# Optimization experiments

Hardware: AMD Instinct MI355X
Metric: run time of the kernel (lower is better)

Reference implementation:

```python
import jax, jax.numpy as jnp
import numpy as np
from jax import lax

DIM = 128
HEADS = 8
B, H, W = 8, 128, 128


def conv1x1(w, x):
    # w: [out_c, in_c], x: [b, in_c, h, w]
    return jnp.einsum('oc,bchw->bohw', w, x)


def setup_inputs() -> dict:
    key = jax.random.key(0)
    ks = jax.random.split(key, 12)
    s = 0.02
    return {
        'x': jax.random.normal(ks[0], (B, DIM, H, W), dtype=jnp.float32),
        'W_qkv': jax.random.normal(ks[1], (3 * DIM, DIM), dtype=jnp.float32) * s,
        'W_dw': jax.random.normal(ks[2], (DIM, 1, 3, 3), dtype=jnp.float32) * s,
        'W_proj_s': jax.random.normal(ks[3], (DIM, DIM), dtype=jnp.float32) * s,
        'scale_s': jnp.ones((HEADS, 1, 1), dtype=jnp.float32),
        'W_ff1': jax.random.normal(ks[4], (DIM, DIM), dtype=jnp.float32) * s,
        'W_ff2': jax.random.normal(ks[5], (DIM, DIM), dtype=jnp.float32) * s,
        'W_proj_f': jax.random.normal(ks[6], (DIM, DIM), dtype=jnp.float32) * s,
        'W_gsf': jax.random.normal(ks[7], (DIM, DIM), dtype=jnp.float32) * s,
        'b_gsf': jnp.zeros((DIM,), dtype=jnp.float32),
        'W_gfs': jax.random.normal(ks[8], (DIM, DIM), dtype=jnp.float32) * s,
        'b_gfs': jnp.zeros((DIM,), dtype=jnp.float32),
    }


def reference(x, W_qkv, W_dw, W_proj_s, scale_s, W_ff1, W_ff2, W_proj_f,
              W_gsf, b_gsf, W_gfs, b_gfs):
    b, c, h, w = x.shape
    head = HEADS
    ch = c // head

    # --- channel self-attention branch ---
    qkv = conv1x1(W_qkv, x)                      # [b, 3c, h, w]
    q_s, k_s, v_s = jnp.split(qkv, 3, axis=1)
    v_s_conv = lax.conv_general_dilated(
        v_s, W_dw, window_strides=(1, 1), padding='SAME',
        feature_group_count=c,
        dimension_numbers=('NCHW', 'OIHW', 'NCHW'))  # depthwise 3x3

    q = q_s.reshape(b, head, ch, h * w)
    k = k_s.reshape(b, head, ch, h * w)
    v = v_s.reshape(b, head, ch, h * w)
    attn = jax.nn.softmax(jnp.einsum('bhcn,bhdn->bhcd', q, k) * scale_s, axis=-1)
    out_s = jnp.einsum('bhcd,bhdn->bhcn', attn, v).reshape(b, c, h, w)
    out_s = conv1x1(W_proj_s, out_s + v_s_conv)

    # --- frequency filter branch ---
    xf = jnp.fft.rfft2(x, norm='ortho')          # complex [b,c,h,w//2+1]
    spatial_weights = conv1x1(W_ff2, jax.nn.gelu(conv1x1(W_ff1, x), approximate=False))
    freq_weights = jnp.fft.rfft2(spatial_weights, norm='ortho')
    out_f = jnp.fft.irfft2(xf * freq_weights, s=(h, w), norm='ortho')
    out_f = conv1x1(W_proj_f, out_f)

    # --- sigmoid-gated fusion ---
    gate_f = jax.nn.sigmoid(conv1x1(W_gsf, out_s) + b_gsf[:, None, None])
    gate_s = jax.nn.sigmoid(conv1x1(W_gfs, out_f) + b_gfs[:, None, None])
    return x + out_s * gate_s + out_f * gate_f
```

## Files before the change

kernel.cpp:

```cpp
#include <hip/hip_runtime.h>
#include <hip/hip_bf16.h>
#include <math.h>

#define HW 16384

typedef __attribute__((ext_vector_type(8))) short bf16x8;
typedef __attribute__((ext_vector_type(4))) float f32x4;

__device__ __forceinline__ unsigned short f2bf(float a)
{
    __hip_bfloat16 h = __float2bfloat16(a);
    return __builtin_bit_cast(unsigned short, h);
}
__device__ __forceinline__ unsigned f2bf_pk(float a, float b)
{
    return (unsigned)f2bf(a) | ((unsigned)f2bf(b) << 16);
}
__device__ __forceinline__ float bf2f(unsigned short u)
{
    return __uint_as_float(((unsigned)u) << 16);
}
__device__ __forceinline__ float sigmoidf_(float v) { return 1.f / (1.f + expf(-v)); }

__device__ __forceinline__ float2 cmul(float2 a, float2 b)
{
    return make_float2(a.x * b.x - a.y * b.y, a.x * b.y + a.y * b.x);
}

__global__ __launch_bounds__(256)
void wprep_k(const float* __restrict__ w0, const float* __restrict__ w1,
             const float* __restrict__ w2, const float* __restrict__ w3,
             const float* __restrict__ w4, const float* __restrict__ w5,
             const float* __restrict__ w6, int4* __restrict__ Wbf4)
{
    int m = blockIdx.x >> 3;
    int slot = (blockIdx.x & 7) * 256 + threadIdx.x;
    const float* src;
    switch (m) {
        case 0: src = w0; break;
        case 1: src = w1; break;
        case 2: src = w2; break;
        case 3: src = w3; break;
        case 4: src = w4; break;
        case 5: src = w5; break;
        default: src = w6; break;
    }
    int o = slot >> 4;
    int c16 = (slot & 15) ^ (o & 7);
    const float* p = src + o * 128 + c16 * 8;
    int4 pk;
    pk.x = f2bf_pk(p[0], p[1]); pk.y = f2bf_pk(p[2], p[3]);
    pk.z = f2bf_pk(p[4], p[5]); pk.w = f2bf_pk(p[6], p[7]);
    Wbf4[m * 2048 + slot] = pk;
}

__global__ __launch_bounds__(256)
void head_k(const float* __restrict__ x, const int4* __restrict__ wv,
            const int4* __restrict__ w1, const int4* __restrict__ w2,
            unsigned short* __restrict__ V, unsigned short* __restrict__ swb,
            unsigned short* __restrict__ xb)
{
    __shared__ short WL[128 * 128];
    __shared__ short XLx[64 * 128];
    __shared__ short XM[64 * 128];
    int t = threadIdx.x;
    int gb = blockIdx.x;
    int b = gb >> 8;
    int n0 = (gb & 255) << 6;

    #pragma unroll
    for (int it = 0; it < 8; ++it)
        ((int4*)WL)[it * 256 + t] = wv[it * 256 + t];

    const float* inb = x + (size_t)b * 128 * HW + n0;
    int nl = t & 63;
    #pragma unroll
    for (int it = 0; it < 4; ++it) {
        int c8 = (t >> 6) + it * 4;
        float v[8];
        unsigned short vb[8];
        #pragma unroll
        for (int j = 0; j < 8; ++j) {
            v[j] = inb[(size_t)(c8 * 8 + j) * HW + nl];
            vb[j] = f2bf(v[j]);
            xb[((size_t)(b * 128) + c8 * 8 + j) * HW + n0 + nl] = vb[j];
        }
        int4 p;
        p.x = (int)((unsigned)vb[0] | ((unsigned)vb[1] << 16));
        p.y = (int)((unsigned)vb[2] | ((unsigned)vb[3] << 16));
        p.z = (int)((unsigned)vb[4] | ((unsigned)vb[5] << 16));
        p.w = (int)((unsigned)vb[6] | ((unsigned)vb[7] << 16));
        ((int4*)XLx)[nl * 16 + (c8 ^ (nl & 7))] = p;
    }
    __syncthreads();

    int l = t & 63, w = t >> 6, kg = l >> 4, l15 = l & 15, l7 = l15 & 7;

    f32x4 acc[2][4];
    #pragma unroll
    for (int mf = 0; mf < 2; ++mf)
        #pragma unroll
        for (int nf = 0; nf < 4; ++nf) acc[mf][nf] = (f32x4){0.f, 0.f, 0.f, 0.f};
    #pragma unroll
    for (int ks = 0; ks < 4; ++ks) {
        int ch = ks * 4 + kg;
        bf16x8 A0 = ((const bf16x8*)WL)[(w * 32 + l15) * 16 + (ch ^ l7)];
        bf16x8 A1 = ((const bf16x8*)WL)[(w * 32 + 16 + l15) * 16 + (ch ^ l7)];
        #pragma unroll
        for (int nf = 0; nf < 4; ++nf) {
            bf16x8 Bf = ((const bf16x8*)XLx)[(nf * 16 + l15) * 16 + (ch ^ l7)];
            acc[0][nf] = __builtin_amdgcn_mfma_f32_16x16x32_bf16(A0, Bf, acc[0][nf], 0, 0, 0);
            acc[1][nf] = __builtin_amdgcn_mfma_f32_16x16x32_bf16(A1, Bf, acc[1][nf], 0, 0, 0);
        }
    }
    #pragma unroll
    for (int mf = 0; mf < 2; ++mf)
        #pragma unroll
        for (int nf = 0; nf < 4; ++nf)
            #pragma unroll
            for (int i = 0; i < 4; ++i) {
                int row = w * 32 + mf * 16 + kg * 4 + i;
                int col = n0 + nf * 16 + l15;
                V[((size_t)b * 128 + row) * HW + col] = f2bf(acc[mf][nf][i]);
            }
    __syncthreads();

    #pragma unroll
    for (int it = 0; it < 8; ++it)
        ((int4*)WL)[it * 256 + t] = w1[it * 256 + t];
    __syncthreads();

    #pragma unroll
    for (int mf = 0; mf < 2; ++mf)
        #pragma unroll
        for (int nf = 0; nf < 4; ++nf) acc[mf][nf] = (f32x4){0.f, 0.f, 0.f, 0.f};
    #pragma unroll
    for (int ks = 0; ks < 4; ++ks) {
        int ch = ks * 4 + kg;
        bf16x8 A0 = ((const bf16x8*)WL)[(w * 32 + l15) * 16 + (ch ^ l7)];
        bf16x8 A1 = ((const bf16x8*)WL)[(w * 32 + 16 + l15) * 16 + (ch ^ l7)];
        #pragma unroll
        for (int nf = 0; nf < 4; ++nf) {
            bf16x8 Bf = ((const bf16x8*)XLx)[(nf * 16 + l15) * 16 + (ch ^ l7)];
            acc[0][nf] = __builtin_amdgcn_mfma_f32_16x16x32_bf16(A0, Bf, acc[0][nf], 0, 0, 0);
            acc[1][nf] = __builtin_amdgcn_mfma_f32_16x16x32_bf16(A1, Bf, acc[1][nf], 0, 0, 0);
        }
    }
    __syncthreads();

    #pragma unroll
    for (int it = 0; it < 8; ++it)
        ((int4*)WL)[it * 256 + t] = w2[it * 256 + t];
    #pragma unroll
    for (int mf = 0; mf < 2; ++mf)
        #pragma unroll
        for (int nf = 0; nf < 4; ++nf) {
            float g4[4];
            #pragma unroll
            for (int i = 0; i < 4; ++i) {
                float v = acc[mf][nf][i];
                g4[i] = 0.5f * v * (1.0f + erff(v * 0.70710678118654752f));
            }
            int col = nf * 16 + l15;
            int r0 = w * 32 + mf * 16 + kg * 4;
            int octet = r0 >> 3;
            uint2 pk2;
            pk2.x = f2bf_pk(g4[0], g4[1]);
            pk2.y = f2bf_pk(g4[2], g4[3]);
            ((uint2*)XM)[(col * 16 + (octet ^ (col & 7))) * 2 + (kg & 1)] = pk2;
        }
    __syncthreads();

    f32x4 acc2[2][4];
    #pragma unroll
    for (int mf = 0; mf < 2; ++mf)
        #pragma unroll
        for (int nf = 0; nf < 4; ++nf) acc2[mf][nf] = (f32x4){0.f, 0.f, 0.f, 0.f};
    #pragma unroll
    for (int ks = 0; ks < 4; ++ks) {
        int ch = ks * 4 + kg;
        bf16x8 A0 = ((const bf16x8*)WL)[(w * 32 + l15) * 16 + (ch ^ l7)];
        bf16x8 A1 = ((const bf16x8*)WL)[(w * 32 + 16 + l15) * 16 + (ch ^ l7)];
        #pragma unroll
        for (int nf = 0; nf < 4; ++nf) {
            bf16x8 Bf = ((const bf16x8*)XM)[(nf * 16 + l15) * 16 + (ch ^ l7)];
            acc2[0][nf] = __builtin_amdgcn_mfma_f32_16x16x32_bf16(A0, Bf, acc2[0][nf], 0, 0, 0);
            acc2[1][nf] = __builtin_amdgcn_mfma_f32_16x16x32_bf16(A1, Bf, acc2[1][nf], 0, 0, 0);
        }
    }
    #pragma unroll
    for (int mf = 0; mf < 2; ++mf)
        #pragma unroll
        for (int nf = 0; nf < 4; ++nf)
            #pragma unroll
            for (int i = 0; i < 4; ++i) {
                int row = w * 32 + mf * 16 + kg * 4 + i;
                int col = n0 + nf * 16 + l15;
                swb[((size_t)b * 128 + row) * HW + col] = f2bf(acc2[mf][nf][i]);
            }
}

__global__ __launch_bounds__(256)
void dwconv_k(const unsigned short* __restrict__ V, const float* __restrict__ Wdw,
              unsigned short* __restrict__ vcb)
{
    __shared__ unsigned short Vt[128 * 128];
    int t = threadIdx.x;
    int bc = blockIdx.x;
    int c = bc & 127;
    const unsigned short* vin = V + (size_t)bc * HW;
    #pragma unroll
    for (int i = 0; i < 16; ++i) {
        int idx = i * 256 + t;
        ((uint2*)Vt)[idx] = ((const uint2*)vin)[idx];
    }
    float wf[9];
    #pragma unroll
    for (int i = 0; i < 9; ++i) wf[i] = Wdw[c * 9 + i];
    __syncthreads();
    #pragma unroll
    for (int i = 0; i < 16; ++i) {
        int q = i * 256 + t;
        int y = q >> 5;
        int x0 = (q & 31) << 2;
        float a0 = 0.f, a1 = 0.f, a2 = 0.f, a3 = 0.f;
        #pragma unroll
        for (int dy = 0; dy < 3; ++dy) {
            int yy = y + dy - 1;
            if (yy < 0 || yy > 127) continue;
            const unsigned short* r = Vt + yy * 128;
            uint2 mu = *(const uint2*)(r + x0);
            float m0 = bf2f((unsigned short)(mu.x & 0xFFFF));
            float m1 = bf2f((unsigned short)(mu.x >> 16));
            float m2 = bf2f((unsigned short)(mu.y & 0xFFFF));
            float m3 = bf2f((unsigned short)(mu.y >> 16));
            float left  = (x0 > 0)   ? bf2f(r[x0 - 1]) : 0.f;
            float right = (x0 < 124) ? bf2f(r[x0 + 4]) : 0.f;
            float w0 = wf[dy * 3], w1 = wf[dy * 3 + 1], w2 = wf[dy * 3 + 2];
            a0 += w0 * left + w1 * m0 + w2 * m1;
            a1 += w0 * m0   + w1 * m1 + w2 * m2;
            a2 += w0 * m1   + w1 * m2 + w2 * m3;
            a3 += w0 * m2   + w1 * m3 + w2 * right;
        }
        uint2 r2;
        r2.x = f2bf_pk(a0, a1);
        r2.y = f2bf_pk(a2, a3);
        *(uint2*)(vcb + (size_t)bc * HW + y * 128 + x0) = r2;
    }
}

__global__ __launch_bounds__(256)
void gram_mfma_k(const unsigned short* __restrict__ xb, float* __restrict__ Gp)
{
    __shared__ short XL[128 * 128];
    int t = threadIdx.x;
    int blk = blockIdx.x;
    int b = blk >> 5, ks = blk & 31;
    const unsigned short* xbb = xb + (size_t)b * 128 * HW + ks * 512;
    int l = t & 63, w = t >> 6, kg = l >> 4, l15 = l & 15, l7 = l15 & 7;

    f32x4 acc[2][8];
    #pragma unroll
    for (int mf = 0; mf < 2; ++mf)
        #pragma unroll
        for (int nf = 0; nf < 8; ++nf) acc[mf][nf] = (f32x4){0.f, 0.f, 0.f, 0.f};

    for (int kc = 0; kc < 4; ++kc) {
        __syncthreads();
        #pragma unroll
        for (int it = 0; it < 8; ++it) {
            int g = it * 256 + t;
            int row = g >> 4, oct = g & 15;
            ((int4*)XL)[row * 16 + (oct ^ (row & 7))] =
                *(const int4*)(xbb + (size_t)row * HW + kc * 128 + oct * 8);
        }
        __syncthreads();
        #pragma unroll
        for (int s = 0; s < 4; ++s) {
            int oct = s * 4 + kg;
            bf16x8 A0 = ((const bf16x8*)XL)[(w * 32 + l15) * 16 + (oct ^ l7)];
            bf16x8 A1 = ((const bf16x8*)XL)[(w * 32 + 16 + l15) * 16 + (oct ^ l7)];
            #pragma unroll
            for (int nf = 0; nf < 8; ++nf) {
                bf16x8 Bf = ((const bf16x8*)XL)[(nf * 16 + l15) * 16 + (oct ^ l7)];
                acc[0][nf] = __builtin_amdgcn_mfma_f32_16x16x32_bf16(A0, Bf, acc[0][nf], 0, 0, 0);
                acc[1][nf] = __builtin_amdgcn_mfma_f32_16x16x32_bf16(A1, Bf, acc[1][nf], 0, 0, 0);
            }
        }
    }
    float* gp = Gp + (size_t)blk * 16384;
    #pragma unroll
    for (int mf = 0; mf < 2; ++mf)
        #pragma unroll
        for (int nf = 0; nf < 8; ++nf)
            #pragma unroll
            for (int i = 0; i < 4; ++i) {
                int row = w * 32 + mf * 16 + kg * 4 + i;
                int col = nf * 16 + l15;
                gp[row * 128 + col] = acc[mf][nf][i];
            }
}

__global__ void gram_reduce_k(const float* __restrict__ Gp, float* __restrict__ G)
{
    int idx = blockIdx.x * 256 + threadIdx.x;
    int b = idx >> 14;
    int ij = idx & 16383;
    const float* gp = Gp + (size_t)(b * 32) * 16384 + ij;
    float s = 0.f;
    #pragma unroll
    for (int ks = 0; ks < 32; ++ks) s += gp[(size_t)ks * 16384];
    G[idx] = s;
}

__global__ __launch_bounds__(256)
void attn_s2_k(const float* __restrict__ G, const float* __restrict__ Wqkv,
               const float* __restrict__ scale, float* __restrict__ S)
{
    __shared__ float Wq[16][129];
    __shared__ float Wk[16][129];
    __shared__ float Ts[16][129];
    int bh = blockIdx.x;
    int b = bh >> 3, h = bh & 7;
    int t = threadIdx.x;
    #pragma unroll
    for (int i = 0; i < 8; ++i) {
        int idx = t + i * 256;
        int r = idx >> 7, ci = idx & 127;
        Wq[r][ci] = Wqkv[(size_t)(h * 16 + r) * 128 + ci];
        Wk[r][ci] = Wqkv[(size_t)(128 + h * 16 + r) * 128 + ci];
    }
    __syncthreads();
    const float* Gb = G + (size_t)b * 16384;
    #pragma unroll
    for (int i = 0; i < 8; ++i) {
        int idx = t + i * 256;
        int c = idx >> 7, col = idx & 127;
        float s = 0.f;
        #pragma unroll 8
        for (int ci = 0; ci < 128; ++ci)
            s += Wq[c][ci] * Gb[ci * 128 + col];
        Ts[c][col] = s;
    }
    __syncthreads();
    int c = t >> 4, d = t & 15;
    float s = 0.f;
    #pragma unroll 8
    for (int col = 0; col < 128; ++col)
        s += Ts[c][col] * Wk[d][col];
    s *= scale[h];
    float m = s;
    #pragma unroll
    for (int w = 1; w < 16; w <<= 1)
        m = fmaxf(m, __shfl_xor(m, w, 64));
    float e = expf(s - m);
    float sum = e;
    #pragma unroll
    for (int w = 1; w < 16; w <<= 1)
        sum += __shfl_xor(sum, w, 64);
    S[(size_t)bh * 256 + t] = e / sum;
}

__global__ __launch_bounds__(256)
void proj_s_pv_k(const unsigned short* __restrict__ V,
                 const unsigned short* __restrict__ vcb,
                 const float* __restrict__ S, const int4* __restrict__ wbf,
                 unsigned short* __restrict__ out_s)
{
    __shared__ short WL[128 * 128];
    __shared__ short XL[64 * 128];
    __shared__ float SL[2048];
    int t = threadIdx.x;
    int gb = blockIdx.x;
    int b = gb >> 8;
    int n0 = (gb & 255) << 6;

    #pragma unroll
    for (int it = 0; it < 8; ++it)
        ((int4*)WL)[it * 256 + t] = wbf[it * 256 + t];
    #pragma unroll
    for (int i = 0; i < 8; ++i)
        SL[i * 256 + t] = S[(size_t)b * 2048 + i * 256 + t];
    __syncthreads();

    int col = t & 63, w = t >> 6;
    #pragma unroll
    for (int hh = 0; hh < 2; ++hh) {
        int h = w * 2 + hh;
        float v[16];
        #pragma unroll
        for (int d = 0; d < 16; ++d)
            v[d] = bf2f(V[((size_t)(b * 128 + h * 16 + d)) * HW + n0 + col]);
        float o[16];
        #pragma unroll
        for (int c = 0; c < 16; ++c) {
            const float* sl = SL + h * 256 + c * 16;
            float s = 0.f;
            #pragma unroll
            for (int d = 0; d < 16; ++d) s += sl[d] * v[d];
            o[c] = s + bf2f(vcb[((size_t)(b * 128 + h * 16 + c)) * HW + n0 + col]);
        }
        #pragma unroll
        for (int oc = 0; oc < 2; ++oc) {
            int octet = h * 2 + oc;
            int4 p;
            p.x = f2bf_pk(o[oc * 8 + 0], o[oc * 8 + 1]);
            p.y = f2bf_pk(o[oc * 8 + 2], o[oc * 8 + 3]);
            p.z = f2bf_pk(o[oc * 8 + 4], o[oc * 8 + 5]);
            p.w = f2bf_pk(o[oc * 8 + 6], o[oc * 8 + 7]);
            ((int4*)XL)[col * 16 + (octet ^ (col & 7))] = p;
        }
    }
    __syncthreads();

    int l = t & 63, kg = l >> 4, l15 = l & 15, l7 = l15 & 7;
    f32x4 acc[2][4];
    #pragma unroll
    for (int mf = 0; mf < 2; ++mf)
        #pragma unroll
        for (int nf = 0; nf < 4; ++nf) acc[mf][nf] = (f32x4){0.f, 0.f, 0.f, 0.f};
    #pragma unroll
    for (int ks = 0; ks < 4; ++ks) {
        int ch = ks * 4 + kg;
        bf16x8 A0 = ((const bf16x8*)WL)[(w * 32 + l15) * 16 + (ch ^ l7)];
        bf16x8 A1 = ((const bf16x8*)WL)[(w * 32 + 16 + l15) * 16 + (ch ^ l7)];
        #pragma unroll
        for (int nf = 0; nf < 4; ++nf) {
            bf16x8 Bf = ((const bf16x8*)XL)[(nf * 16 + l15) * 16 + (ch ^ l7)];
            acc[0][nf] = __builtin_amdgcn_mfma_f32_16x16x32_bf16(A0, Bf, acc[0][nf], 0, 0, 0);
            acc[1][nf] = __builtin_amdgcn_mfma_f32_16x16x32_bf16(A1, Bf, acc[1][nf], 0, 0, 0);
        }
    }
    #pragma unroll
    for (int mf = 0; mf < 2; ++mf)
        #pragma unroll
        for (int nf = 0; nf < 4; ++nf)
            #pragma unroll
            for (int i = 0; i < 4; ++i) {
                int row = w * 32 + mf * 16 + kg * 4 + i;
                int colg = n0 + nf * 16 + l15;
                out_s[((size_t)b * 128 + row) * HW + colg] = f2bf(acc[mf][nf][i]);
            }
}

__global__ __launch_bounds__(256)
void tail_k(const float* __restrict__ x, const unsigned short* __restrict__ outs,
            const unsigned short* __restrict__ pre,
            const int4* __restrict__ wpf,
            const int4* __restrict__ wgsf, const float* __restrict__ bgsf,
            const int4* __restrict__ wgfs, const float* __restrict__ bgfs,
            float* __restrict__ out)
{
    __shared__ short WL[128 * 128];
    __shared__ short XP[64 * 128];
    __shared__ short XS[64 * 128];
    int t = threadIdx.x;
    int gb = blockIdx.x;
    int T = (gb & 7) * 256 + (gb >> 3);
    int b = T >> 8;
    int n0 = (T & 255) << 6;

    #pragma unroll
    for (int it = 0; it < 8; ++it)
        ((int4*)WL)[it * 256 + t] = wpf[it * 256 + t];

    const unsigned short* pb = pre + (size_t)b * 128 * HW + n0;
    const unsigned short* sb = outs + (size_t)b * 128 * HW + n0;
    int nl = t & 63;
    #pragma unroll
    for (int it = 0; it < 4; ++it) {
        int c8 = (t >> 6) + it * 4;
        unsigned up[8], us[8];
        #pragma unroll
        for (int j = 0; j < 8; ++j) {
            size_t a = (size_t)(c8 * 8 + j) * HW + nl;
            up[j] = pb[a];
            us[j] = sb[a];
        }
        int4 pp, ps;
        pp.x = (int)(up[0] | (up[1] << 16)); pp.y = (int)(up[2] | (up[3] << 16));
        pp.z = (int)(up[4] | (up[5] << 16)); pp.w = (int)(up[6] | (up[7] << 16));
        ps.x = (int)(us[0] | (us[1] << 16)); ps.y = (int)(us[2] | (us[3] << 16));
        ps.z = (int)(us[4] | (us[5] << 16)); ps.w = (int)(us[6] | (us[7] << 16));
        ((int4*)XP)[nl * 16 + (c8 ^ (nl & 7))] = pp;
        ((int4*)XS)[nl * 16 + (c8 ^ (nl & 7))] = ps;
    }
    __syncthreads();

    int l = t & 63, w = t >> 6, kg = l >> 4, l15 = l & 15, l7 = l15 & 7;

    f32x4 accF[2][4];
    #pragma unroll
    for (int mf = 0; mf < 2; ++mf)
        #pragma unroll
        for (int nf = 0; nf < 4; ++nf) accF[mf][nf] = (f32x4){0.f, 0.f, 0.f, 0.f};
    #pragma unroll
    for (int ks = 0; ks < 4; ++ks) {
        int ch = ks * 4 + kg;
        bf16x8 A0 = ((const bf16x8*)WL)[(w * 32 + l15) * 16 + (ch ^ l7)];
        bf16x8 A1 = ((const bf16x8*)WL)[(w * 32 + 16 + l15) * 16 + (ch ^ l7)];
        #pragma unroll
        for (int nf = 0; nf < 4; ++nf) {
            bf16x8 Bf = ((const bf16x8*)XP)[(nf * 16 + l15) * 16 + (ch ^ l7)];
            accF[0][nf] = __builtin_amdgcn_mfma_f32_16x16x32_bf16(A0, Bf, accF[0][nf], 0, 0, 0);
            accF[1][nf] = __builtin_amdgcn_mfma_f32_16x16x32_bf16(A1, Bf, accF[1][nf], 0, 0, 0);
        }
    }
    __syncthreads();

    #pragma unroll
    for (int it = 0; it < 8; ++it)
        ((int4*)WL)[it * 256 + t] = wgsf[it * 256 + t];
    #pragma unroll
    for (int mf = 0; mf < 2; ++mf)
        #pragma unroll
        for (int nf = 0; nf < 4; ++nf) {
            int col = nf * 16 + l15;
            int r0 = w * 32 + mf * 16 + kg * 4;
            int octet = r0 >> 3;
            uint2 pk2;
            pk2.x = f2bf_pk(accF[mf][nf][0], accF[mf][nf][1]);
            pk2.y = f2bf_pk(accF[mf][nf][2], accF[mf][nf][3]);
            ((uint2*)XP)[(col * 16 + (octet ^ (col & 7))) * 2 + (kg & 1)] = pk2;
        }
    __syncthreads();

    f32x4 aS[2][4];
    #pragma unroll
    for (int mf = 0; mf < 2; ++mf)
        #pragma unroll
        for (int nf = 0; nf < 4; ++nf) aS[mf][nf] = (f32x4){0.f, 0.f, 0.f, 0.f};
    #pragma unroll
    for (int ks = 0; ks < 4; ++ks) {
        int ch = ks * 4 + kg;
        bf16x8 A0 = ((const bf16x8*)WL)[(w * 32 + l15) * 16 + (ch ^ l7)];
        bf16x8 A1 = ((const bf16x8*)WL)[(w * 32 + 16 + l15) * 16 + (ch ^ l7)];
        #pragma unroll
        for (int nf = 0; nf < 4; ++nf) {
            bf16x8 Bf = ((const bf16x8*)XS)[(nf * 16 + l15) * 16 + (ch ^ l7)];
            aS[0][nf] = __builtin_amdgcn_mfma_f32_16x16x32_bf16(A0, Bf, aS[0][nf], 0, 0, 0);
            aS[1][nf] = __builtin_amdgcn_mfma_f32_16x16x32_bf16(A1, Bf, aS[1][nf], 0, 0, 0);
        }
    }
    __syncthreads();

    #pragma unroll
    for (int it = 0; it < 8; ++it)
        ((int4*)WL)[it * 256 + t] = wgfs[it * 256 + t];
    __syncthreads();

    f32x4 aF[2][4];
    #pragma unroll
    for (int mf = 0; mf < 2; ++mf)
        #pragma unroll
        for (int nf = 0; nf < 4; ++nf) aF[mf][nf] = (f32x4){0.f, 0.f, 0.f, 0.f};
    #pragma unroll
    for (int ks = 0; ks < 4; ++ks) {
        int ch = ks * 4 + kg;
        bf16x8 A0 = ((const bf16x8*)WL)[(w * 32 + l15) * 16 + (ch ^ l7)];
        bf16x8 A1 = ((const bf16x8*)WL)[(w * 32 + 16 + l15) * 16 + (ch ^ l7)];
        #pragma unroll
        for (int nf = 0; nf < 4; ++nf) {
            bf16x8 Bf = ((const bf16x8*)XP)[(nf * 16 + l15) * 16 + (ch ^ l7)];
            aF[0][nf] = __builtin_amdgcn_mfma_f32_16x16x32_bf16(A0, Bf, aF[0][nf], 0, 0, 0);
            aF[1][nf] = __builtin_amdgcn_mfma_f32_16x16x32_bf16(A1, Bf, aF[1][nf], 0, 0, 0);
        }
    }

    #pragma unroll
    for (int mf = 0; mf < 2; ++mf)
        #pragma unroll
        for (int nf = 0; nf < 4; ++nf)
            #pragma unroll
            for (int i = 0; i < 4; ++i) {
                int row = w * 32 + mf * 16 + kg * 4 + i;
                int cc = n0 + nf * 16 + l15;
                float gf = sigmoidf_(aS[mf][nf][i] + bgsf[row]);
                float gs = sigmoidf_(aF[mf][nf][i] + bgfs[row]);
                size_t gi = ((size_t)(b * 128) + row) * HW + cc;
                float os = bf2f(outs[gi]);
                float of = accF[mf][nf][i];
                out[gi] = x[gi] + os * gs + of * gf;
            }
}

__device__ __forceinline__ int ZIX(int r, int j)
{
    return r * 128 + (j ^ (((r ^ (r >> 4)) & 3) << 3) ^ (((j >> 4) & 3) << 1));
}
__device__ __forceinline__ float2 zld(const unsigned* Z, int r, int j)
{
    unsigned z = Z[ZIX(r, j)];
    return make_float2(bf2f((unsigned short)(z & 0xFFFF)),
                       bf2f((unsigned short)(z >> 16)));
}
__device__ __forceinline__ void zst(unsigned* Z, int r, int j, float2 v)
{
    Z[ZIX(r, j)] = f2bf_pk(v.x, v.y);
}

__device__ __forceinline__ void dft16(float2* v)
{
    const float C1 = 0.92387953251f, S1 = 0.38268343236f, R2 = 0.70710678119f;
    const float2 W16[8] = {
        {1.f, 0.f}, {C1, -S1}, {R2, -R2}, {S1, -C1},
        {0.f, -1.f}, {-S1, -C1}, {-R2, -R2}, {-C1, -S1}};
    #pragma unroll
    for (int i = 0; i < 8; ++i) {
        float2 a = v[i], b = v[i + 8];
        v[i] = make_float2(a.x + b.x, a.y + b.y);
        float2 d = make_float2(a.x - b.x, a.y - b.y);
        v[i + 8] = cmul(d, W16[i]);
    }
    #pragma unroll
    for (int blk = 0; blk < 16; blk += 8)
        #pragma unroll
        for (int i = 0; i < 4; ++i) {
            float2 a = v[blk + i], b = v[blk + i + 4];
            v[blk + i] = make_float2(a.x + b.x, a.y + b.y);
            float2 d = make_float2(a.x - b.x, a.y - b.y);
            v[blk + i + 4] = cmul(d, W16[2 * i]);
        }
    #pragma unroll
    for (int blk = 0; blk < 16; blk += 4) {
        float2 a0 = v[blk], b0 = v[blk + 2];
        v[blk] = make_float2(a0.x + b0.x, a0.y + b0.y);
        v[blk + 2] = make_float2(a0.x - b0.x, a0.y - b0.y);
        float2 a1 = v[blk + 1], b1 = v[blk + 3];
        v[blk + 1] = make_float2(a1.x + b1.x, a1.y + b1.y);
        float2 d = make_float2(a1.x - b1.x, a1.y - b1.y);
        v[blk + 3] = make_float2(d.y, -d.x);
    }
    #pragma unroll
    for (int blk = 0; blk < 16; blk += 2) {
        float2 a = v[blk], b = v[blk + 1];
        v[blk] = make_float2(a.x + b.x, a.y + b.y);
        v[blk + 1] = make_float2(a.x - b.x, a.y - b.y);
    }
}

__device__ __forceinline__ void dft8(float2* v)
{
    const float R2 = 0.70710678119f;
    const float2 W8[4] = {{1.f, 0.f}, {R2, -R2}, {0.f, -1.f}, {-R2, -R2}};
    #pragma unroll
    for (int i = 0; i < 4; ++i) {
        float2 a = v[i], b = v[i + 4];
        v[i] = make_float2(a.x + b.x, a.y + b.y);
        float2 d = make_float2(a.x - b.x, a.y - b.y);
        v[i + 4] = cmul(d, W8[i]);
    }
    #pragma unroll
    for (int blk = 0; blk < 8; blk += 4) {
        float2 a0 = v[blk], b0 = v[blk + 2];
        v[blk] = make_float2(a0.x + b0.x, a0.y + b0.y);
        v[blk + 2] = make_float2(a0.x - b0.x, a0.y - b0.y);
        float2 a1 = v[blk + 1], b1 = v[blk + 3];
        v[blk + 1] = make_float2(a1.x + b1.x, a1.y + b1.y);
        float2 d = make_float2(a1.x - b1.x, a1.y - b1.y);
        v[blk + 3] = make_float2(d.y, -d.x);
    }
    #pragma unroll
    for (int blk = 0; blk < 8; blk += 2) {
        float2 a = v[blk], b = v[blk + 1];
        v[blk] = make_float2(a.x + b.x, a.y + b.y);
        v[blk + 1] = make_float2(a.x - b.x, a.y - b.y);
    }
}

__device__ __forceinline__ void fft_line_row(unsigned* Z, const float2* tw,
                                             int row, int n2)
{
    const int BREV4[16] = {0,8,4,12,2,10,6,14,1,9,5,13,3,11,7,15};
    const int BREV3[8] = {0,4,2,6,1,5,3,7};
    float2 v[16];
    #pragma unroll
    for (int n1 = 0; n1 < 16; ++n1) v[n1] = zld(Z, row, 8 * n1 + n2);
    dft16(v);
    #pragma unroll
    for (int p = 0; p < 16; ++p) {
        int k1 = BREV4[p];
        zst(Z, row, 16 * n2 + k1, cmul(v[p], tw[n2 * k1]));
    }
    float2 wa[8], wb[8];
    #pragma unroll
    for (int m = 0; m < 8; ++m) {
        wa[m] = zld(Z, row, 16 * m + n2);
        wb[m] = zld(Z, row, 16 * m + n2 + 8);
    }
    dft8(wa);
    dft8(wb);
    #pragma unroll
    for (int p = 0; p < 8; ++p) {
        zst(Z, row, n2 + 16 * BREV3[p], wa[p]);
        zst(Z, row, n2 + 8 + 16 * BREV3[p], wb[p]);
    }
}

__device__ __forceinline__ void fft_line_col(unsigned* Z, const float2* tw,
                                             int col, int n2)
{
    const int BREV4[16] = {0,8,4,12,2,10,6,14,1,9,5,13,3,11,7,15};
    const int BREV3[8] = {0,4,2,6,1,5,3,7};
    float2 v[16];
    #pragma unroll
    for (int n1 = 0; n1 < 16; ++n1) v[n1] = zld(Z, 8 * n1 + n2, col);
    dft16(v);
    #pragma unroll
    for (int p = 0; p < 16; ++p) {
        int k1 = BREV4[p];
        zst(Z, 16 * n2 + k1, col, cmul(v[p], tw[n2 * k1]));
    }
    float2 wa[8], wb[8];
    #pragma unroll
    for (int m = 0; m < 8; ++m) {
        wa[m] = zld(Z, 16 * m + n2, col);
        wb[m] = zld(Z, 16 * m + n2 + 8, col);
    }
    dft8(wa);
    dft8(wb);
    #pragma unroll
    for (int p = 0; p < 8; ++p) {
        zst(Z, n2 + 16 * BREV3[p], col, wa[p]);
        zst(Z, n2 + 8 + 16 * BREV3[p], col, wb[p]);
    }
}

__global__ __launch_bounds__(256)
void fft_all_k(const unsigned short* __restrict__ xb,
               const unsigned short* __restrict__ sw,
               unsigned short* __restrict__ outp)
{
    __shared__ unsigned Z[128 * 128];
    __shared__ float2 tw[128];
    const int BREV3[8] = {0,4,2,6,1,5,3,7};
    int t = threadIdx.x;
    if (t < 128) {
        float sn, cs;
        sincosf(0.049087385212340519f * (float)t, &sn, &cs);
        tw[t] = make_float2(cs, -sn);
    }
    size_t base = (size_t)blockIdx.x * HW;

    #pragma unroll
    for (int i = 0; i < 16; ++i) {
        int idx4 = (i * 256 + t) * 4;
        int r = idx4 >> 7, j = idx4 & 127;
        uint2 xv = *(const uint2*)(xb + base + idx4);
        uint2 sv = *(const uint2*)(sw + base + idx4);
        Z[ZIX(r, j + 0)] = (xv.x & 0xFFFFu) | (sv.x << 16);
        Z[ZIX(r, j + 1)] = (xv.x >> 16)     | (sv.x & 0xFFFF0000u);
        Z[ZIX(r, j + 2)] = (xv.y & 0xFFFFu) | (sv.y << 16);
        Z[ZIX(r, j + 3)] = (xv.y >> 16)     | (sv.y & 0xFFFF0000u);
    }
    __syncthreads();

    int ln = t >> 3, n2 = t & 7;
    #pragma unroll
    for (int it = 0; it < 4; ++it) fft_line_row(Z, tw, it * 32 + ln, n2);
    __syncthreads();
    #pragma unroll
    for (int it = 0; it < 4; ++it) fft_line_col(Z, tw, it * 32 + ln, n2);
    __syncthreads();

    for (int item = t; item < 8194; item += 256) {
        int rA, kA, rB, kB;
        if (item < 8064) {
            rA = 1 + (item >> 7); kA = item & 127;
            rB = 128 - rA; kB = (128 - kA) & 127;
        } else {
            int it2 = item - 8064;
            rA = rB = (it2 < 65) ? 0 : 64;
            kA = (it2 < 65) ? it2 : (it2 - 65);
            kB = (128 - kA) & 127;
        }
        float2 z1 = zld(Z, rA, kA);
        float2 z2 = zld(Z, rB, kB);
        float2 X = make_float2(0.5f * (z1.x + z2.x), 0.5f * (z1.y - z2.y));
        float Dx = z1.x - z2.x, Dy = z1.y + z2.y;
        float2 Wf = make_float2(0.5f * Dy, -0.5f * Dx);
        float2 Y = cmul(X, Wf);
        zst(Z, rA, kA, make_float2(Y.x, -Y.y));
        zst(Z, rB, kB, Y);
    }
    __syncthreads();

    #pragma unroll
    for (int it = 0; it < 4; ++it) fft_line_col(Z, tw, it * 32 + ln, n2);
    __syncthreads();

    const float scale = 1.f / 2097152.f;
    const int BREV4[16] = {0,8,4,12,2,10,6,14,1,9,5,13,3,11,7,15};
    #pragma unroll
    for (int it = 0; it < 4; ++it) {
        int row = it * 32 + ln;
        float2 v[16];
        #pragma unroll
        for (int n1 = 0; n1 < 16; ++n1) v[n1] = zld(Z, row, 8 * n1 + n2);
        dft16(v);
        #pragma unroll
        for (int p = 0; p < 16; ++p) {
            int k1 = BREV4[p];
            zst(Z, row, 16 * n2 + k1, cmul(v[p], tw[n2 * k1]));
        }
        float2 wa[8], wb[8];
        #pragma unroll
        for (int m = 0; m < 8; ++m) {
            wa[m] = zld(Z, row, 16 * m + n2);
            wb[m] = zld(Z, row, 16 * m + n2 + 8);
        }
        dft8(wa);
        dft8(wb);
        #pragma unroll
        for (int p = 0; p < 8; ++p) {
            outp[base + row * 128 + n2 + 16 * BREV3[p]] = f2bf(wa[p].x * scale);
            outp[base + row * 128 + n2 + 8 + 16 * BREV3[p]] = f2bf(wb[p].x * scale);
        }
    }
}

extern "C" void kernel_launch(void* const* d_in, const int* in_sizes, int n_in,
                              void* d_out, int out_size, void* d_ws, size_t ws_size,
                              hipStream_t stream)
{
    const float* x        = (const float*)d_in[0];
    const float* W_qkv    = (const float*)d_in[1];
    const float* W_dw     = (const float*)d_in[2];
    const float* W_proj_s = (const float*)d_in[3];
    const float* scale_s  = (const float*)d_in[4];
    const float* W_ff1    = (const float*)d_in[5];
    const float* W_ff2    = (const float*)d_in[6];
    const float* W_proj_f = (const float*)d_in[7];
    const float* W_gsf    = (const float*)d_in[8];
    const float* b_gsf    = (const float*)d_in[9];
    const float* W_gfs    = (const float*)d_in[10];
    const float* b_gfs    = (const float*)d_in[11];
    float* out = (float*)d_out;

    char* ws = (char*)d_ws;
    const size_t MB32 = 33554432ull;
    const size_t MB64 = 67108864ull;
    const size_t MB96 = 100663296ull;
    const size_t MB97 = 101711872ull;
    unsigned short* V     = (unsigned short*)(ws);
    unsigned short* out_s = (unsigned short*)(ws + MB32);
    unsigned short* swb   = (unsigned short*)(ws + MB64);
    unsigned short* pre   = (unsigned short*)(ws + MB64);
    int4* Wbf4            = (int4*)(ws + MB96);
    float* Gp  = (float*)(ws + MB97);
    float* G   = Gp + 4194304;
    float* S   = G + 131072;
    unsigned short* vcb = (unsigned short*)out;
    unsigned short* xb  = (unsigned short*)out + 16777216;

    wprep_k<<<56, 256, 0, stream>>>(W_qkv + 256 * 128, W_proj_s, W_ff1, W_ff2,
                                    W_proj_f, W_gsf, W_gfs, Wbf4);

    head_k<<<2048, 256, 0, stream>>>(x, Wbf4 + 0 * 2048, Wbf4 + 2 * 2048,
                                     Wbf4 + 3 * 2048, V, swb, xb);

    dwconv_k<<<1024, 256, 0, stream>>>(V, W_dw, vcb);
    gram_mfma_k<<<256, 256, 0, stream>>>(xb, Gp);
    gram_reduce_k<<<512, 256, 0, stream>>>(Gp, G);
    attn_s2_k<<<64, 256, 0, stream>>>(G, W_qkv, scale_s, S);
    proj_s_pv_k<<<2048, 256, 0, stream>>>(V, vcb, S, Wbf4 + 1 * 2048, out_s);

    fft_all_k<<<1024, 256, 0, stream>>>(xb, swb, pre);

    tail_k<<<2048, 256, 0, stream>>>(x, out_s, pre, Wbf4 + 4 * 2048,
                                     Wbf4 + 5 * 2048, b_gsf,
                                     Wbf4 + 6 * 2048, b_gfs, out);
}
```

Before: 286.0 us.

## Fuse FFT, depthwise conv and Gram kernels into one mixed-role launch

The separate dwconv, Gram-partial and FFT-filter kernels are merged into a single mid_k launch. It dispatches on blockIdx: each group of 9 blocks runs 4 FFT channels, 4 depthwise-conv channels and 1 Gram partial. These three stages are mutually independent, so the fusion removes two launches and the tails between them and lets them overlap on the GPU. The cost is that every block now reserves the FFT-sized shared-memory buffer and the union of register needs. That can lower occupancy for the lighter dwconv and Gram roles.

```diff
diff --git a/kernel.cpp b/kernel.cpp
--- a/kernel.cpp
+++ b/kernel.cpp
@@ -200,13 +200,248 @@
             }
 }
 
-__global__ __launch_bounds__(256)
-void dwconv_k(const unsigned short* __restrict__ V, const float* __restrict__ Wdw,
-              unsigned short* __restrict__ vcb)
-{
-    __shared__ unsigned short Vt[128 * 128];
+__device__ __forceinline__ int ZIX(int r, int j)
+{
+    return r * 128 + (j ^ (((r ^ (r >> 4)) & 3) << 3) ^ (((j >> 4) & 3) << 1));
+}
+__device__ __forceinline__ float2 zld(const unsigned* Z, int r, int j)
+{
+    unsigned z = Z[ZIX(r, j)];
+    return make_float2(bf2f((unsigned short)(z & 0xFFFF)),
+                       bf2f((unsigned short)(z >> 16)));
+}
+__device__ __forceinline__ void zst(unsigned* Z, int r, int j, float2 v)
+{
+    Z[ZIX(r, j)] = f2bf_pk(v.x, v.y);
+}
+
+__device__ __forceinline__ void dft16(float2* v)
+{
+    const float C1 = 0.92387953251f, S1 = 0.38268343236f, R2 = 0.70710678119f;
+    const float2 W16[8] = {
+        {1.f, 0.f}, {C1, -S1}, {R2, -R2}, {S1, -C1},
+        {0.f, -1.f}, {-S1, -C1}, {-R2, -R2}, {-C1, -S1}};
+    #pragma unroll
+    for (int i = 0; i < 8; ++i) {
+        float2 a = v[i], b = v[i + 8];
+        v[i] = make_float2(a.x + b.x, a.y + b.y);
+        float2 d = make_float2(a.x - b.x, a.y - b.y);
+        v[i + 8] = cmul(d, W16[i]);
+    }
+    #pragma unroll
+    for (int blk = 0; blk < 16; blk += 8)
+        #pragma unroll
+        for (int i = 0; i < 4; ++i) {
+            float2 a = v[blk + i], b = v[blk + i + 4];
+            v[blk + i] = make_float2(a.x + b.x, a.y + b.y);
+            float2 d = make_float2(a.x - b.x, a.y - b.y);
+            v[blk + i + 4] = cmul(d, W16[2 * i]);
+        }
+    #pragma unroll
+    for (int blk = 0; blk < 16; blk += 4) {
+        float2 a0 = v[blk], b0 = v[blk + 2];
+        v[blk] = make_float2(a0.x + b0.x, a0.y + b0.y);
+        v[blk + 2] = make_float2(a0.x - b0.x, a0.y - b0.y);
+        float2 a1 = v[blk + 1], b1 = v[blk + 3];
+        v[blk + 1] = make_float2(a1.x + b1.x, a1.y + b1.y);
+        float2 d = make_float2(a1.x - b1.x, a1.y - b1.y);
+        v[blk + 3] = make_float2(d.y, -d.x);
+    }
+    #pragma unroll
+    for (int blk = 0; blk < 16; blk += 2) {
+        float2 a = v[blk], b = v[blk + 1];
+        v[blk] = make_float2(a.x + b.x, a.y + b.y);
+        v[blk + 1] = make_float2(a.x - b.x, a.y - b.y);
+    }
+}
+
+__device__ __forceinline__ void dft8(float2* v)
+{
+    const float R2 = 0.70710678119f;
+    const float2 W8[4] = {{1.f, 0.f}, {R2, -R2}, {0.f, -1.f}, {-R2, -R2}};
+    #pragma unroll
+    for (int i = 0; i < 4; ++i) {
+        float2 a = v[i], b = v[i + 4];
+        v[i] = make_float2(a.x + b.x, a.y + b.y);
+        float2 d = make_float2(a.x - b.x, a.y - b.y);
+        v[i + 4] = cmul(d, W8[i]);
+    }
+    #pragma unroll
+    for (int blk = 0; blk < 8; blk += 4) {
+        float2 a0 = v[blk], b0 = v[blk + 2];
+        v[blk] = make_float2(a0.x + b0.x, a0.y + b0.y);
+        v[blk + 2] = make_float2(a0.x - b0.x, a0.y - b0.y);
+        float2 a1 = v[blk + 1], b1 = v[blk + 3];
+        v[blk + 1] = make_float2(a1.x + b1.x, a1.y + b1.y);
+        float2 d = make_float2(a1.x - b1.x, a1.y - b1.y);
+        v[blk + 3] = make_float2(d.y, -d.x);
+    }
+    #pragma unroll
+    for (int blk = 0; blk < 8; blk += 2) {
+        float2 a = v[blk], b = v[blk + 1];
+        v[blk] = make_float2(a.x + b.x, a.y + b.y);
+        v[blk + 1] = make_float2(a.x - b.x, a.y - b.y);
+    }
+}
+
+__device__ __forceinline__ void fft_line_row(unsigned* Z, const float2* tw,
+                                             int row, int n2)
+{
+    const int BREV4[16] = {0,8,4,12,2,10,6,14,1,9,5,13,3,11,7,15};
+    const int BREV3[8] = {0,4,2,6,1,5,3,7};
+    float2 v[16];
+    #pragma unroll
+    for (int n1 = 0; n1 < 16; ++n1) v[n1] = zld(Z, row, 8 * n1 + n2);
+    dft16(v);
+    #pragma unroll
+    for (int p = 0; p < 16; ++p) {
+        int k1 = BREV4[p];
+        zst(Z, row, 16 * n2 + k1, cmul(v[p], tw[n2 * k1]));
+    }
+    float2 wa[8], wb[8];
+    #pragma unroll
+    for (int m = 0; m < 8; ++m) {
+        wa[m] = zld(Z, row, 16 * m + n2);
+        wb[m] = zld(Z, row, 16 * m + n2 + 8);
+    }
+    dft8(wa);
+    dft8(wb);
+    #pragma unroll
+    for (int p = 0; p < 8; ++p) {
+        zst(Z, row, n2 + 16 * BREV3[p], wa[p]);
+        zst(Z, row, n2 + 8 + 16 * BREV3[p], wb[p]);
+    }
+}
+
+__device__ __forceinline__ void fft_line_col(unsigned* Z, const float2* tw,
+                                             int col, int n2)
+{
+    const int BREV4[16] = {0,8,4,12,2,10,6,14,1,9,5,13,3,11,7,15};
+    const int BREV3[8] = {0,4,2,6,1,5,3,7};
+    float2 v[16];
+    #pragma unroll
+    for (int n1 = 0; n1 < 16; ++n1) v[n1] = zld(Z, 8 * n1 + n2, col);
+    dft16(v);
+    #pragma unroll
+    for (int p = 0; p < 16; ++p) {
+        int k1 = BREV4[p];
+        zst(Z, 16 * n2 + k1, col, cmul(v[p], tw[n2 * k1]));
+    }
+    float2 wa[8], wb[8];
+    #pragma unroll
+    for (int m = 0; m < 8; ++m) {
+        wa[m] = zld(Z, 16 * m + n2, col);
+        wb[m] = zld(Z, 16 * m + n2 + 8, col);
+    }
+    dft8(wa);
+    dft8(wb);
+    #pragma unroll
+    for (int p = 0; p < 8; ++p) {
+        zst(Z, n2 + 16 * BREV3[p], col, wa[p]);
+        zst(Z, n2 + 8 + 16 * BREV3[p], col, wb[p]);
+    }
+}
+
+__device__ void fft_body(char* smem, int ch,
+                         const unsigned short* __restrict__ xb,
+                         const unsigned short* __restrict__ sw,
+                         unsigned short* __restrict__ outp)
+{
+    unsigned* Z = (unsigned*)smem;
+    float2* tw = (float2*)(smem + 65536);
+    const int BREV3[8] = {0,4,2,6,1,5,3,7};
     int t = threadIdx.x;
-    int bc = blockIdx.x;
+    if (t < 128) {
+        float sn, cs;
+        sincosf(0.049087385212340519f * (float)t, &sn, &cs);
+        tw[t] = make_float2(cs, -sn);
+    }
+    size_t base = (size_t)ch * HW;
+
+    #pragma unroll
+    for (int i = 0; i < 16; ++i) {
+        int idx4 = (i * 256 + t) * 4;
+        int r = idx4 >> 7, j = idx4 & 127;
+        uint2 xv = *(const uint2*)(xb + base + idx4);
+        uint2 sv = *(const uint2*)(sw + base + idx4);
+        Z[ZIX(r, j + 0)] = (xv.x & 0xFFFFu) | (sv.x << 16);
+        Z[ZIX(r, j + 1)] = (xv.x >> 16)     | (sv.x & 0xFFFF0000u);
+        Z[ZIX(r, j + 2)] = (xv.y & 0xFFFFu) | (sv.y << 16);
+        Z[ZIX(r, j + 3)] = (xv.y >> 16)     | (sv.y & 0xFFFF0000u);
+    }
+    __syncthreads();
+
+    int ln = t >> 3, n2 = t & 7;
+    #pragma unroll
+    for (int it = 0; it < 4; ++it) fft_line_row(Z, tw, it * 32 + ln, n2);
+    __syncthreads();
+    #pragma unroll
+    for (int it = 0; it < 4; ++it) fft_line_col(Z, tw, it * 32 + ln, n2);
+    __syncthreads();
+
+    for (int item = t; item < 8194; item += 256) {
+        int rA, kA, rB, kB;
+        if (item < 8064) {
+            rA = 1 + (item >> 7); kA = item & 127;
+            rB = 128 - rA; kB = (128 - kA) & 127;
+        } else {
+            int it2 = item - 8064;
+            rA = rB = (it2 < 65) ? 0 : 64;
+            kA = (it2 < 65) ? it2 : (it2 - 65);
+            kB = (128 - kA) & 127;
+        }
+        float2 z1 = zld(Z, rA, kA);
+        float2 z2 = zld(Z, rB, kB);
+        float2 X = make_float2(0.5f * (z1.x + z2.x), 0.5f * (z1.y - z2.y));
+        float Dx = z1.x - z2.x, Dy = z1.y + z2.y;
+        float2 Wf = make_float2(0.5f * Dy, -0.5f * Dx);
+        float2 Y = cmul(X, Wf);
+        zst(Z, rA, kA, make_float2(Y.x, -Y.y));
+        zst(Z, rB, kB, Y);
+    }
+    __syncthreads();
+
+    #pragma unroll
+    for (int it = 0; it < 4; ++it) fft_line_col(Z, tw, it * 32 + ln, n2);
+    __syncthreads();
+
+    const float scale = 1.f / 2097152.f;
+    const int BREV4[16] = {0,8,4,12,2,10,6,14,1,9,5,13,3,11,7,15};
+    #pragma unroll
+    for (int it = 0; it < 4; ++it) {
+        int row = it * 32 + ln;
+        float2 v[16];
+        #pragma unroll
+        for (int n1 = 0; n1 < 16; ++n1) v[n1] = zld(Z, row, 8 * n1 + n2);
+        dft16(v);
+        #pragma unroll
+        for (int p = 0; p < 16; ++p) {
+            int k1 = BREV4[p];
+            zst(Z, row, 16 * n2 + k1, cmul(v[p], tw[n2 * k1]));
+        }
+        float2 wa[8], wb[8];
+        #pragma unroll
+        for (int m = 0; m < 8; ++m) {
+            wa[m] = zld(Z, row, 16 * m + n2);
+            wb[m] = zld(Z, row, 16 * m + n2 + 8);
+        }
+        dft8(wa);
+        dft8(wb);
+        #pragma unroll
+        for (int p = 0; p < 8; ++p) {
+            outp[base + row * 128 + n2 + 16 * BREV3[p]] = f2bf(wa[p].x * scale);
+            outp[base + row * 128 + n2 + 8 + 16 * BREV3[p]] = f2bf(wb[p].x * scale);
+        }
+    }
+}
+
+__device__ void dwconv_body(char* smem, int bc,
+                            const unsigned short* __restrict__ V,
+                            const float* __restrict__ Wdw,
+                            unsigned short* __restrict__ vcb)
+{
+    unsigned short* Vt = (unsigned short*)smem;
+    int t = threadIdx.x;
     int c = bc & 127;
     const unsigned short* vin = V + (size_t)bc * HW;
     #pragma unroll
@@ -249,12 +484,12 @@
     }
 }
 
-__global__ __launch_bounds__(256)
-void gram_mfma_k(const unsigned short* __restrict__ xb, float* __restrict__ Gp)
-{
-    __shared__ short XL[128 * 128];
+__device__ void gram_body(char* smem, int blk,
+                          const unsigned short* __restrict__ xb,
+                          float* __restrict__ Gp)
+{
+    short* XL = (short*)smem;
     int t = threadIdx.x;
-    int blk = blockIdx.x;
     int b = blk >> 5, ks = blk & 31;
     const unsigned short* xbb = xb + (size_t)b * 128 * HW + ks * 512;
     int l = t & 63, w = t >> 6, kg = l >> 4, l15 = l & 15, l7 = l15 & 7;
@@ -299,6 +534,22 @@
                 int col = nf * 16 + l15;
                 gp[row * 128 + col] = acc[mf][nf][i];
             }
+}
+
+__global__ __launch_bounds__(256)
+void mid_k(const unsigned short* __restrict__ xb,
+           const unsigned short* __restrict__ swb,
+           unsigned short* __restrict__ pre,
+           const unsigned short* __restrict__ V,
+           const float* __restrict__ Wdw, unsigned short* __restrict__ vcb,
+           float* __restrict__ Gp)
+{
+    __shared__ __align__(16) char smem[66560];
+    int bid = blockIdx.x;
+    int g = bid / 9, s = bid - g * 9;
+    if (s < 4)       fft_body(smem, g * 4 + s, xb, swb, pre);
+    else if (s < 8)  dwconv_body(smem, g * 4 + (s - 4), V, Wdw, vcb);
+    else             gram_body(smem, g, xb, Gp);
 }
 
 __global__ void gram_reduce_k(const float* __restrict__ Gp, float* __restrict__ G)
@@ -582,241 +833,6 @@
                 float of = accF[mf][nf][i];
                 out[gi] = x[gi] + os * gs + of * gf;
             }
-}
-
-__device__ __forceinline__ int ZIX(int r, int j)
-{
-    return r * 128 + (j ^ (((r ^ (r >> 4)) & 3) << 3) ^ (((j >> 4) & 3) << 1));
-}
-__device__ __forceinline__ float2 zld(const unsigned* Z, int r, int j)
-{
-    unsigned z = Z[ZIX(r, j)];
-    return make_float2(bf2f((unsigned short)(z & 0xFFFF)),
-                       bf2f((unsigned short)(z >> 16)));
-}
-__device__ __forceinline__ void zst(unsigned* Z, int r, int j, float2 v)
-{
-    Z[ZIX(r, j)] = f2bf_pk(v.x, v.y);
-}
-
-__device__ __forceinline__ void dft16(float2* v)
-{
-    const float C1 = 0.92387953251f, S1 = 0.38268343236f, R2 = 0.70710678119f;
-    const float2 W16[8] = {
-        {1.f, 0.f}, {C1, -S1}, {R2, -R2}, {S1, -C1},
-        {0.f, -1.f}, {-S1, -C1}, {-R2, -R2}, {-C1, -S1}};
-    #pragma unroll
-    for (int i = 0; i < 8; ++i) {
-        float2 a = v[i], b = v[i + 8];
-        v[i] = make_float2(a.x + b.x, a.y + b.y);
-        float2 d = make_float2(a.x - b.x, a.y - b.y);
-        v[i + 8] = cmul(d, W16[i]);
-    }
-    #pragma unroll
-    for (int blk = 0; blk < 16; blk += 8)
-        #pragma unroll
-        for (int i = 0; i < 4; ++i) {
-            float2 a = v[blk + i], b = v[blk + i + 4];
-            v[blk + i] = make_float2(a.x + b.x, a.y + b.y);
-            float2 d = make_float2(a.x - b.x, a.y - b.y);
-            v[blk + i + 4] = cmul(d, W16[2 * i]);
-        }
-    #pragma unroll
-    for (int blk = 0; blk < 16; blk += 4) {
-        float2 a0 = v[blk], b0 = v[blk + 2];
-        v[blk] = make_float2(a0.x + b0.x, a0.y + b0.y);
-        v[blk + 2] = make_float2(a0.x - b0.x, a0.y - b0.y);
-        float2 a1 = v[blk + 1], b1 = v[blk + 3];
-        v[blk + 1] = make_float2(a1.x + b1.x, a1.y + b1.y);
-        float2 d = make_float2(a1.x - b1.x, a1.y - b1.y);
-        v[blk + 3] = make_float2(d.y, -d.x);
-    }
-    #pragma unroll
-    for (int blk = 0; blk < 16; blk += 2) {
-        float2 a = v[blk], b = v[blk + 1];
-        v[blk] = make_float2(a.x + b.x, a.y + b.y);
-        v[blk + 1] = make_float2(a.x - b.x, a.y - b.y);
-    }
-}
-
-__device__ __forceinline__ void dft8(float2* v)
-{
-    const float R2 = 0.70710678119f;
-    const float2 W8[4] = {{1.f, 0.f}, {R2, -R2}, {0.f, -1.f}, {-R2, -R2}};
-    #pragma unroll
-    for (int i = 0; i < 4; ++i) {
-        float2 a = v[i], b = v[i + 4];
-        v[i] = make_float2(a.x + b.x, a.y + b.y);
-        float2 d = make_float2(a.x - b.x, a.y - b.y);
-        v[i + 4] = cmul(d, W8[i]);
-    }
-    #pragma unroll
-    for (int blk = 0; blk < 8; blk += 4) {
-        float2 a0 = v[blk], b0 = v[blk + 2];
-        v[blk] = make_float2(a0.x + b0.x, a0.y + b0.y);
-        v[blk + 2] = make_float2(a0.x - b0.x, a0.y - b0.y);
-        float2 a1 = v[blk + 1], b1 = v[blk + 3];
-        v[blk + 1] = make_float2(a1.x + b1.x, a1.y + b1.y);
-        float2 d = make_float2(a1.x - b1.x, a1.y - b1.y);
-        v[blk + 3] = make_float2(d.y, -d.x);
-    }
-    #pragma unroll
-    for (int blk = 0; blk < 8; blk += 2) {
-        float2 a = v[blk], b = v[blk + 1];
-        v[blk] = make_float2(a.x + b.x, a.y + b.y);
-        v[blk + 1] = make_float2(a.x - b.x, a.y - b.y);
-    }
-}
-
-__device__ __forceinline__ void fft_line_row(unsigned* Z, const float2* tw,
-                                             int row, int n2)
-{
-    const int BREV4[16] = {0,8,4,12,2,10,6,14,1,9,5,13,3,11,7,15};
-    const int BREV3[8] = {0,4,2,6,1,5,3,7};
-    float2 v[16];
-    #pragma unroll
-    for (int n1 = 0; n1 < 16; ++n1) v[n1] = zld(Z, row, 8 * n1 + n2);
-    dft16(v);
-    #pragma unroll
-    for (int p = 0; p < 16; ++p) {
-        int k1 = BREV4[p];
-        zst(Z, row, 16 * n2 + k1, cmul(v[p], tw[n2 * k1]));
-    }
-    float2 wa[8], wb[8];
-    #pragma unroll
-    for (int m = 0; m < 8; ++m) {
-        wa[m] = zld(Z, row, 16 * m + n2);
-        wb[m] = zld(Z, row, 16 * m + n2 + 8);
-    }
-    dft8(wa);
-    dft8(wb);
-    #pragma unroll
-    for (int p = 0; p < 8; ++p) {
-        zst(Z, row, n2 + 16 * BREV3[p], wa[p]);
-        zst(Z, row, n2 + 8 + 16 * BREV3[p], wb[p]);
-    }
-}
-
-__device__ __forceinline__ void fft_line_col(unsigned* Z, const float2* tw,
-                                             int col, int n2)
-{
-    const int BREV4[16] = {0,8,4,12,2,10,6,14,1,9,5,13,3,11,7,15};
-    const int BREV3[8] = {0,4,2,6,1,5,3,7};
-    float2 v[16];
-    #pragma unroll
-    for (int n1 = 0; n1 < 16; ++n1) v[n1] = zld(Z, 8 * n1 + n2, col);
-    dft16(v);
-    #pragma unroll
-    for (int p = 0; p < 16; ++p) {
-        int k1 = BREV4[p];
-        zst(Z, 16 * n2 + k1, col, cmul(v[p], tw[n2 * k1]));
-    }
-    float2 wa[8], wb[8];
-    #pragma unroll
-    for (int m = 0; m < 8; ++m) {
-        wa[m] = zld(Z, 16 * m + n2, col);
-        wb[m] = zld(Z, 16 * m + n2 + 8, col);
-    }
-    dft8(wa);
-    dft8(wb);
-    #pragma unroll
-    for (int p = 0; p < 8; ++p) {
-        zst(Z, n2 + 16 * BREV3[p], col, wa[p]);
-        zst(Z, n2 + 8 + 16 * BREV3[p], col, wb[p]);
-    }
-}
-
-__global__ __launch_bounds__(256)
-void fft_all_k(const unsigned short* __restrict__ xb,
-               const unsigned short* __restrict__ sw,
-               unsigned short* __restrict__ outp)
-{
-    __shared__ unsigned Z[128 * 128];
-    __shared__ float2 tw[128];
-    const int BREV3[8] = {0,4,2,6,1,5,3,7};
-    int t = threadIdx.x;
-    if (t < 128) {
-        float sn, cs;
-        sincosf(0.049087385212340519f * (float)t, &sn, &cs);
-        tw[t] = make_float2(cs, -sn);
-    }
-    size_t base = (size_t)blockIdx.x * HW;
-
-    #pragma unroll
-    for (int i = 0; i < 16; ++i) {
-        int idx4 = (i * 256 + t) * 4;
-        int r = idx4 >> 7, j = idx4 & 127;
-        uint2 xv = *(const uint2*)(xb + base + idx4);
-        uint2 sv = *(const uint2*)(sw + base + idx4);
-        Z[ZIX(r, j + 0)] = (xv.x & 0xFFFFu) | (sv.x << 16);
-        Z[ZIX(r, j + 1)] = (xv.x >> 16)     | (sv.x & 0xFFFF0000u);
-        Z[ZIX(r, j + 2)] = (xv.y & 0xFFFFu) | (sv.y << 16);
-        Z[ZIX(r, j + 3)] = (xv.y >> 16)     | (sv.y & 0xFFFF0000u);
-    }
-    __syncthreads();
-
-    int ln = t >> 3, n2 = t & 7;
-    #pragma unroll
-    for (int it = 0; it < 4; ++it) fft_line_row(Z, tw, it * 32 + ln, n2);
-    __syncthreads();
-    #pragma unroll
-    for (int it = 0; it < 4; ++it) fft_line_col(Z, tw, it * 32 + ln, n2);
-    __syncthreads();
-
-    for (int item = t; item < 8194; item += 256) {
-        int rA, kA, rB, kB;
-        if (item < 8064) {
-            rA = 1 + (item >> 7); kA = item & 127;
-            rB = 128 - rA; kB = (128 - kA) & 127;
-        } else {
-            int it2 = item - 8064;
-            rA = rB = (it2 < 65) ? 0 : 64;
-            kA = (it2 < 65) ? it2 : (it2 - 65);
-            kB = (128 - kA) & 127;
-        }
-        float2 z1 = zld(Z, rA, kA);
-        float2 z2 = zld(Z, rB, kB);
-        float2 X = make_float2(0.5f * (z1.x + z2.x), 0.5f * (z1.y - z2.y));
-        float Dx = z1.x - z2.x, Dy = z1.y + z2.y;
-        float2 Wf = make_float2(0.5f * Dy, -0.5f * Dx);
-        float2 Y = cmul(X, Wf);
-        zst(Z, rA, kA, make_float2(Y.x, -Y.y));
-        zst(Z, rB, kB, Y);
-    }
-    __syncthreads();
-
-    #pragma unroll
-    for (int it = 0; it < 4; ++it) fft_line_col(Z, tw, it * 32 + ln, n2);
-    __syncthreads();
-
-    const float scale = 1.f / 2097152.f;
-    const int BREV4[16] = {0,8,4,12,2,10,6,14,1,9,5,13,3,11,7,15};
-    #pragma unroll
-    for (int it = 0; it < 4; ++it) {
-        int row = it * 32 + ln;
-        float2 v[16];
-        #pragma unroll
-        for (int n1 = 0; n1 < 16; ++n1) v[n1] = zld(Z, row, 8 * n1 + n2);
-        dft16(v);
-        #pragma unroll
-        for (int p = 0; p < 16; ++p) {
-            int k1 = BREV4[p];
-            zst(Z, row, 16 * n2 + k1, cmul(v[p], tw[n2 * k1]));
-        }
-        float2 wa[8], wb[8];
-        #pragma unroll
-        for (int m = 0; m < 8; ++m) {
-            wa[m] = zld(Z, row, 16 * m + n2);
-            wb[m] = zld(Z, row, 16 * m + n2 + 8);
-        }
-        dft8(wa);
-        dft8(wb);
-        #pragma unroll
-        for (int p = 0; p < 8; ++p) {
-            outp[base + row * 128 + n2 + 16 * BREV3[p]] = f2bf(wa[p].x * scale);
-            outp[base + row * 128 + n2 + 8 + 16 * BREV3[p]] = f2bf(wb[p].x * scale);
-        }
-    }
 }
 
 extern "C" void kernel_launch(void* const* d_in, const int* in_sizes, int n_in,
@@ -859,14 +875,12 @@
     head_k<<<2048, 256, 0, stream>>>(x, Wbf4 + 0 * 2048, Wbf4 + 2 * 2048,
                                      Wbf4 + 3 * 2048, V, swb, xb);
 
-    dwconv_k<<<1024, 256, 0, stream>>>(V, W_dw, vcb);
-    gram_mfma_k<<<256, 256, 0, stream>>>(xb, Gp);
+    mid_k<<<2304, 256, 0, stream>>>(xb, swb, pre, V, W_dw, vcb, Gp);
+
     gram_reduce_k<<<512, 256, 0, stream>>>(Gp, G);
     attn_s2_k<<<64, 256, 0, stream>>>(G, W_qkv, scale_s, S);
     proj_s_pv_k<<<2048, 256, 0, stream>>>(V, vcb, S, Wbf4 + 1 * 2048, out_s);
 
-    fft_all_k<<<1024, 256, 0, stream>>>(xb, swb, pre);
-
     tail_k<<<2048, 256, 0, stream>>>(x, out_s, pre, Wbf4 + 4 * 2048,
                                      Wbf4 + 5 * 2048, b_gsf,
                                      Wbf4 + 6 * 2048, b_gfs, out);
```

After: 357.6 us. 1.25x slower.
